# Kernel optimization log

Measured on AMD Instinct MI355X. Metric: run time of the kernel, lower is better.

The kernel has to match this reference:

```python
import jax, jax.numpy as jnp
import numpy as np

VOCAB = 50257
EMB = 512
HID = 512


def setup_inputs() -> dict:
    key = jax.random.key(0)
    ks = jax.random.split(key, 8)
    x = jax.random.randint(ks[0], (64, 512), 0, VOCAB, dtype=jnp.int32)
    emb = jax.random.normal(ks[1], (VOCAB, EMB), dtype=jnp.float32) * 0.02
    # stacked LSTM gate weights per layer: order (i, f, o, c); Linear(in=EMB+HID or HID+HID, out=HID)
    s0 = 1.0 / np.sqrt(EMB + HID)
    s1 = 1.0 / np.sqrt(HID + HID)
    W0 = jax.random.uniform(ks[2], (4, HID, EMB + HID), jnp.float32, -s0, s0)
    b0 = jax.random.uniform(ks[3], (4, HID), jnp.float32, -s0, s0)
    W1 = jax.random.uniform(ks[4], (4, HID, HID + HID), jnp.float32, -s1, s1)
    b1 = jax.random.uniform(ks[5], (4, HID), jnp.float32, -s1, s1)
    sf = 1.0 / np.sqrt(HID)
    fc_w = jax.random.uniform(ks[6], (1, HID), jnp.float32, -sf, sf)
    fc_b = jax.random.uniform(ks[7], (1,), jnp.float32, -sf, sf)
    return {"x": x, "emb": emb, "W0": W0, "b0": b0, "W1": W1, "b1": b1,
            "fc_w": fc_w, "fc_b": fc_b}


def _lstm_cell(inp, h, c, W, b):
    # combined = [inp, h]; gates stacked (i, f, o, c); activation = relu
    combined = jnp.concatenate([inp, h], axis=-1)        # [B, In+H]
    gates = jnp.einsum('bi,ghi->bgh', combined, W) + b   # [B, 4, H]
    i_t = jax.nn.sigmoid(gates[:, 0])
    f_t = jax.nn.sigmoid(gates[:, 1])
    o_t = jax.nn.sigmoid(gates[:, 2])
    g_t = jax.nn.relu(gates[:, 3])
    c_new = f_t * c + i_t * g_t
    h_new = o_t * jax.nn.relu(c_new)
    return h_new, c_new


def reference(x, emb, W0, b0, W1, b1, fc_w, fc_b):
    B, T = x.shape
    emb_z = emb.at[0].set(0.0)          # padding_idx=0
    xe = emb_z[x]                        # [B, T, EMB]
    xe = jnp.transpose(xe, (1, 0, 2))    # [T, B, EMB]

    def step(carry, x_t):
        h0, c0, h1, c1 = carry
        h0, c0 = _lstm_cell(x_t, h0, c0, W0, b0)
        h1, c1 = _lstm_cell(h0, h1, c1, W1, b1)
        return (h0, c0, h1, c1), None

    z = jnp.zeros((B, HID), dtype=xe.dtype)
    (h0, c0, h1, c1), _ = jax.lax.scan(step, (z, z, z, z), xe)
    out = h1 @ fc_w.T + fc_b             # [B, 1]
    return jax.nn.sigmoid(out)
```

## Files before the change

kernel.cpp:

```cpp
#include <hip/hip_runtime.h>
#include <hip/hip_bf16.h>
#include <math.h>

typedef __attribute__((ext_vector_type(8))) short bf16x8;
typedef __attribute__((ext_vector_type(4))) float f32x4;

static constexpr int Tc = 512, HIDc = 512;
static constexpr int NWGc = 256, THR = 256;

static constexpr size_t WSB_H0  = 0;
static constexpr size_t WSB_H1  = WSB_H0 + 3ull * 65536;
static constexpr size_t WSB_XE  = WSB_H1 + 2ull * 65536;
static constexpr size_t WSB_CTR = WSB_XE + 3ull * 65536;
static constexpr size_t WSB_EPO = WSB_CTR + 512;
static constexpr size_t WSB_FLG = WSB_EPO + 64;
static constexpr size_t WSB_END = WSB_FLG + 256 * 64;

static constexpr unsigned FMAGIC = 0x1357acedu;
static constexpr unsigned EPBASE = 0x40000000u;

__device__ __forceinline__ unsigned ld_devu(const unsigned* p) {
    return __hip_atomic_load(p, __ATOMIC_RELAXED, __HIP_MEMORY_SCOPE_AGENT);
}
__device__ __forceinline__ unsigned long long ld_devu64(const unsigned long long* p) {
    return __hip_atomic_load(p, __ATOMIC_RELAXED, __HIP_MEMORY_SCOPE_AGENT);
}
__device__ __forceinline__ void st_devu(unsigned* p, unsigned v) {
    __hip_atomic_store(p, v, __ATOMIC_RELAXED, __HIP_MEMORY_SCOPE_AGENT);
}
template<int N> __device__ __forceinline__ void s_wait_vm() {
    asm volatile("s_waitcnt vmcnt(%0)" :: "n"(N) : "memory");
}
__device__ __forceinline__ void s_wait_lgkm() {
    asm volatile("s_waitcnt lgkmcnt(0)" ::: "memory");
}
__device__ __forceinline__ void wgbar() {
    asm volatile("" ::: "memory");
    __builtin_amdgcn_s_barrier();
    asm volatile("" ::: "memory");
}
__device__ __forceinline__ unsigned short bfc(float f) {
    __hip_bfloat16 h = __float2bfloat16(f);
    return *(unsigned short*)&h;
}
__device__ __forceinline__ float bf2f(unsigned short u) {
    __hip_bfloat16 h; *(unsigned short*)&h = u;
    return __bfloat162float(h);
}

__global__ __launch_bounds__(THR, 1)
void lstm_persistent(const int* __restrict__ xp,
                     const float* __restrict__ emb,
                     const float* __restrict__ W0,
                     const float* __restrict__ b0,
                     const float* __restrict__ W1,
                     const float* __restrict__ b1,
                     const float* __restrict__ fcw,
                     const float* __restrict__ fcb,
                     float* __restrict__ out,
                     float* __restrict__ ws)
{
    char* wsc = (char*)ws;

    unsigned* ctr = (unsigned*)(wsc + WSB_CTR);
    unsigned* epo = (unsigned*)(wsc + WSB_EPO);
    unsigned* flg = (unsigned*)(wsc + WSB_FLG);

    __shared__ float preF[16 * 68];
    __shared__ float hexF[4 * 64];

    const int  tid   = threadIdx.x;
    const int  wg    = blockIdx.x;
    const bool is_l0 = (wg < 128);
    const int  hw    = (is_l0 ? wg : wg - 128) * 4;
    const float* Wb  = is_l0 ? W0 : W1;
    const float* bb  = is_l0 ? b0 : b1;
    const int  b_    = tid & 63;
    const int  wv    = __builtin_amdgcn_readfirstlane(tid >> 6);
    const int  n = tid & 15;
    const int  q = (tid & 63) >> 4;
    const size_t rowB = (size_t)(wv * 16 + n) * 1024 + (size_t)q * 16;

    if (wg == 0 && tid < 64) out[tid] = 0.25f;

    {
        unsigned long long* hz = (unsigned long long*)(wsc + WSB_H0);
        const int i = wg * THR + tid;
        if (i < 5 * 8192)
            __hip_atomic_store(hz + i, 0ull, __ATOMIC_RELAXED, __HIP_MEMORY_SCOPE_AGENT);
    }

    const int be = wg >> 1;
    const int p2 = ((wg & 1) << 7) + (tid & 127);
    auto emb_produce = [&](int wn) {
        if (tid < 128) {
            const int tok = xp[be * Tc + wn];
            float2 v = make_float2(0.f, 0.f);
            if (tok) v = *(const float2*)(emb + (size_t)tok * 512 + p2 * 2);
            unsigned u = (unsigned)bfc(v.x) | ((unsigned)bfc(v.y) << 16);
            st_devu((unsigned*)(wsc + WSB_XE + (size_t)(wn % 3) * 65536) + be * 256 + p2, u);
        }
    };
    if (is_l0) { emb_produce(0); emb_produce(1); }

    bf16x8 bw[32];
    {
        const float* wrow = Wb + (size_t)((n >> 2) * HIDc + hw + (n & 3)) * 1024;
        #pragma unroll
        for (int f = 0; f < 32; ++f) {
            const int k0 = f * 32 + q * 8;
            const float4 u0 = *(const float4*)(wrow + k0);
            const float4 u1 = *(const float4*)(wrow + k0 + 4);
            union { unsigned short us[8]; bf16x8 v; } pk;
            pk.us[0] = bfc(u0.x); pk.us[1] = bfc(u0.y);
            pk.us[2] = bfc(u0.z); pk.us[3] = bfc(u0.w);
            pk.us[4] = bfc(u1.x); pk.us[5] = bfc(u1.y);
            pk.us[6] = bfc(u1.z); pk.us[7] = bfc(u1.w);
            bw[f] = pk.v;
        }
    }
    const float bias_n = bb[(n >> 2) * HIDc + hw + (n & 3)];

    s_wait_vm<0>();
    wgbar();
    if (tid == 0) st_devu(&flg[wg * 16], FMAGIC);
    if (wg == 0 && tid == 0) {
        for (int g = 0; g < NWGc; ++g) {
            while (ld_devu(&flg[g * 16]) != FMAGIC) __builtin_amdgcn_s_sleep(1);
        }
        #pragma unroll
        for (int g = 0; g < 8; ++g) st_devu(&ctr[g * 16], 0u);
        s_wait_vm<0>();
        st_devu(epo, EPBASE);
    } else if (tid == 0) {
        while (ld_devu(epo) != EPBASE) __builtin_amdgcn_s_sleep(1);
    }
    wgbar();

    float cpriv = 0.0f;

    auto ldfrag = [&](const char* slab, int cloc, int s) -> bf16x8 {
        const unsigned long long* p =
            (const unsigned long long*)(slab + rowB + (size_t)cloc * 256 + (size_t)s * 64);
        union { unsigned long long u[2]; bf16x8 v; } r;
        r.u[0] = ld_devu64(p);
        r.u[1] = ld_devu64(p + 1);
        return r.v;
    };

    #pragma unroll 1
    for (int w = 0; w <= Tc + 1; ++w) {
        const bool a0  = is_l0 && (w < Tc);
        const bool a1  = !is_l0 && (w >= 2);
        const bool act = a0 || a1;

        bf16x8 fa[16];
        if (act) {
            const char* slabA = is_l0
                ? (wsc + WSB_XE + (size_t)(w % 3) * 65536)
                : (wsc + WSB_H0 + (size_t)((w - 2) % 3) * 65536);
            #pragma unroll
            for (int c = 0; c < 4; ++c) {
                #pragma unroll
                for (int s = 0; s < 4; ++s)
                    fa[c * 4 + s] = ldfrag(slabA, c, s);
            }
        }

        if (wg == 0) {
            if (tid == 0) {
                const unsigned tgt = (unsigned)NWGc * (unsigned)w;
                for (;;) {
                    unsigned s = 0;
                    #pragma unroll
                    for (int g = 0; g < 8; ++g) s += ld_devu(&ctr[g * 16]);
                    if (s >= tgt) break;
                }
                st_devu(epo, EPBASE + 1u + (unsigned)w);
            }
        } else {
            if (tid == 0) {
                while (ld_devu(epo) < EPBASE + 1u + (unsigned)w)
                    __builtin_amdgcn_s_sleep(1);
            }
        }
        wgbar();

        if (act) {
            const char* slabB = is_l0
                ? (wsc + WSB_H0 + (size_t)((w + 2) % 3) * 65536)
                : (wsc + WSB_H1 + (size_t)((w - 3) & 1) * 65536);
            bf16x8 fb[16];
            #pragma unroll
            for (int c = 0; c < 4; ++c) {
                #pragma unroll
                for (int s = 0; s < 4; ++s)
                    fb[c * 4 + s] = ldfrag(slabB, c, s);
            }

            f32x4 acc = {0.f, 0.f, 0.f, 0.f};
            #pragma unroll
            for (int i = 0; i < 16; ++i)
                acc = __builtin_amdgcn_mfma_f32_16x16x32_bf16(fa[i], bw[i], acc, 0, 0, 0);
            #pragma unroll
            for (int i = 0; i < 16; ++i)
                acc = __builtin_amdgcn_mfma_f32_16x16x32_bf16(fb[i], bw[16 + i], acc, 0, 0, 0);

            *(f32x4*)(preF + (size_t)n * 68 + wv * 16 + q * 4) = acc + bias_n;
            s_wait_lgkm(); wgbar();

            const float pI = preF[(0 * 4 + wv) * 68 + b_];
            const float pF = preF[(1 * 4 + wv) * 68 + b_];
            const float pO = preF[(2 * 4 + wv) * 68 + b_];
            const float pG = preF[(3 * 4 + wv) * 68 + b_];
            const float ig = 1.f / (1.f + expf(-pI));
            const float fg = 1.f / (1.f + expf(-pF));
            const float og = 1.f / (1.f + expf(-pO));
            const float gg = fmaxf(pG, 0.f);
            cpriv = fg * cpriv + ig * gg;
            const float hn = og * fmaxf(cpriv, 0.f);
            hexF[wv * 64 + b_] = hn;
            s_wait_lgkm(); wgbar();

            if (tid < 64) {
                unsigned long long pk = 0;
                #pragma unroll
                for (int jj = 0; jj < 4; ++jj)
                    pk |= (unsigned long long)bfc(hexF[jj * 64 + tid]) << (16 * jj);
                unsigned short* hdst = is_l0
                    ? (unsigned short*)(wsc + WSB_H0 + (size_t)(w % 3) * 65536)
                    : (unsigned short*)(wsc + WSB_H1 + (size_t)((w - 2) & 1) * 65536);
                __hip_atomic_store((unsigned long long*)(hdst + (size_t)tid * 512 + hw),
                                   pk, __ATOMIC_RELAXED, __HIP_MEMORY_SCOPE_AGENT);
            }
        }

        if (is_l0 && (w + 2) < Tc) emb_produce(w + 2);

        s_wait_vm<0>();
        wgbar();
        if (tid == 0)
            __hip_atomic_fetch_add(&ctr[(wg & 7) * 16], 1u, __ATOMIC_RELAXED,
                                   __HIP_MEMORY_SCOPE_AGENT);
    }

    if (wg == 0) {
        if (tid == 0) {
            const unsigned tgt = (unsigned)NWGc * (unsigned)(Tc + 2);
            for (;;) {
                unsigned s = 0;
                #pragma unroll
                for (int g = 0; g < 8; ++g) s += ld_devu(&ctr[g * 16]);
                if (s >= tgt) break;
            }
        }
        wgbar();
        if (tid < 64) {
            const unsigned short* h1f =
                (const unsigned short*)(wsc + WSB_H1 + (size_t)((Tc - 1) & 1) * 65536)
                + (size_t)tid * 512;
            float s = fcb[0];
            for (int h = 0; h < HIDc; h += 4) {
                const unsigned long long u = ld_devu64((const unsigned long long*)(h1f + h));
                s = fmaf(bf2f((unsigned short)(u        & 0xffff)), fcw[h + 0], s);
                s = fmaf(bf2f((unsigned short)((u >> 16) & 0xffff)), fcw[h + 1], s);
                s = fmaf(bf2f((unsigned short)((u >> 32) & 0xffff)), fcw[h + 2], s);
                s = fmaf(bf2f((unsigned short)((u >> 48) & 0xffff)), fcw[h + 3], s);
            }
            out[tid] = 1.f / (1.f + expf(-s));
        }
    }
}

extern "C" void kernel_launch(void* const* d_in, const int* in_sizes, int n_in,
                              void* d_out, int out_size, void* d_ws, size_t ws_size,
                              hipStream_t stream) {
    const int*   xp  = (const int*)d_in[0];
    const float* emb = (const float*)d_in[1];
    const float* W0  = (const float*)d_in[2];
    const float* b0  = (const float*)d_in[3];
    const float* W1  = (const float*)d_in[4];
    const float* b1  = (const float*)d_in[5];
    const float* fcw = (const float*)d_in[6];
    const float* fcb = (const float*)d_in[7];
    float* out = (float*)d_out;
    float* ws  = (float*)d_ws;

    if (ws_size < WSB_END) return;

    lstm_persistent<<<dim3(NWGc), dim3(THR), 0, stream>>>(
        xp, emb, W0, b0, W1, b1, fcw, fcb, out, ws);
}
```

Baseline: 5.133 ms.

## Overlap input-half MFMAs and embedding gather with grid barrier wait

Moves the 16 MFMAs over the input slab (embedding or layer-0 h) ahead of the grid-wide epoch barrier, so they run while waiting for other workgroups. The embedding gather for step w+2 is also issued before the barrier and stored after it, which takes its global load latency off the critical path at the end of the step. It also adds iteration caps to every spin-wait loop. A cap that triggers would silently break synchronisation instead of hanging.

```diff
diff --git a/kernel.cpp b/kernel.cpp
--- a/kernel.cpp
+++ b/kernel.cpp
@@ -18,6 +18,7 @@
 
 static constexpr unsigned FMAGIC = 0x1357acedu;
 static constexpr unsigned EPBASE = 0x40000000u;
+static constexpr int SPIN_CAP = 1 << 20;
 
 __device__ __forceinline__ unsigned ld_devu(const unsigned* p) {
     return __hip_atomic_load(p, __ATOMIC_RELAXED, __HIP_MEMORY_SCOPE_AGENT);
@@ -92,16 +93,21 @@
 
     const int be = wg >> 1;
     const int p2 = ((wg & 1) << 7) + (tid & 127);
-    auto emb_produce = [&](int wn) {
+    auto emb_gather = [&](int wn) -> float2 {
+        float2 v = make_float2(0.f, 0.f);
         if (tid < 128) {
             const int tok = xp[be * Tc + wn];
-            float2 v = make_float2(0.f, 0.f);
             if (tok) v = *(const float2*)(emb + (size_t)tok * 512 + p2 * 2);
+        }
+        return v;
+    };
+    auto emb_store = [&](int wn, float2 v) {
+        if (tid < 128) {
             unsigned u = (unsigned)bfc(v.x) | ((unsigned)bfc(v.y) << 16);
             st_devu((unsigned*)(wsc + WSB_XE + (size_t)(wn % 3) * 65536) + be * 256 + p2, u);
         }
     };
-    if (is_l0) { emb_produce(0); emb_produce(1); }
+    if (is_l0) { emb_store(0, emb_gather(0)); emb_store(1, emb_gather(1)); }
 
     bf16x8 bw[32];
     {
@@ -126,14 +132,18 @@
     if (tid == 0) st_devu(&flg[wg * 16], FMAGIC);
     if (wg == 0 && tid == 0) {
         for (int g = 0; g < NWGc; ++g) {
-            while (ld_devu(&flg[g * 16]) != FMAGIC) __builtin_amdgcn_s_sleep(1);
+            int gu = 0;
+            while (ld_devu(&flg[g * 16]) != FMAGIC && ++gu < SPIN_CAP)
+                __builtin_amdgcn_s_sleep(1);
         }
         #pragma unroll
         for (int g = 0; g < 8; ++g) st_devu(&ctr[g * 16], 0u);
         s_wait_vm<0>();
         st_devu(epo, EPBASE);
     } else if (tid == 0) {
-        while (ld_devu(epo) != EPBASE) __builtin_amdgcn_s_sleep(1);
+        int gu = 0;
+        while (ld_devu(epo) != EPBASE && ++gu < SPIN_CAP)
+            __builtin_amdgcn_s_sleep(1);
     }
     wgbar();
 
@@ -154,37 +164,50 @@
         const bool a1  = !is_l0 && (w >= 2);
         const bool act = a0 || a1;
 
-        bf16x8 fa[16];
+        f32x4 acc = {0.f, 0.f, 0.f, 0.f};
+
         if (act) {
             const char* slabA = is_l0
                 ? (wsc + WSB_XE + (size_t)(w % 3) * 65536)
                 : (wsc + WSB_H0 + (size_t)((w - 2) % 3) * 65536);
+            bf16x8 fa[16];
             #pragma unroll
             for (int c = 0; c < 4; ++c) {
                 #pragma unroll
                 for (int s = 0; s < 4; ++s)
                     fa[c * 4 + s] = ldfrag(slabA, c, s);
             }
-        }
+            #pragma unroll
+            for (int i = 0; i < 16; ++i)
+                acc = __builtin_amdgcn_mfma_f32_16x16x32_bf16(fa[i], bw[i], acc, 0, 0, 0);
+        }
+
+        const bool ep = is_l0 && (w + 2) < Tc;
+        float2 ev = make_float2(0.f, 0.f);
+        if (ep) ev = emb_gather(w + 2);
 
         if (wg == 0) {
             if (tid == 0) {
                 const unsigned tgt = (unsigned)NWGc * (unsigned)w;
+                int gu = 0;
                 for (;;) {
                     unsigned s = 0;
                     #pragma unroll
                     for (int g = 0; g < 8; ++g) s += ld_devu(&ctr[g * 16]);
-                    if (s >= tgt) break;
+                    if (s >= tgt || ++gu >= SPIN_CAP) break;
                 }
                 st_devu(epo, EPBASE + 1u + (unsigned)w);
             }
         } else {
             if (tid == 0) {
-                while (ld_devu(epo) < EPBASE + 1u + (unsigned)w)
+                int gu = 0;
+                while (ld_devu(epo) < EPBASE + 1u + (unsigned)w && ++gu < SPIN_CAP)
                     __builtin_amdgcn_s_sleep(1);
             }
         }
         wgbar();
+
+        if (ep) emb_store(w + 2, ev);
 
         if (act) {
             const char* slabB = is_l0
@@ -197,11 +220,6 @@
                 for (int s = 0; s < 4; ++s)
                     fb[c * 4 + s] = ldfrag(slabB, c, s);
             }
-
-            f32x4 acc = {0.f, 0.f, 0.f, 0.f};
-            #pragma unroll
-            for (int i = 0; i < 16; ++i)
-                acc = __builtin_amdgcn_mfma_f32_16x16x32_bf16(fa[i], bw[i], acc, 0, 0, 0);
             #pragma unroll
             for (int i = 0; i < 16; ++i)
                 acc = __builtin_amdgcn_mfma_f32_16x16x32_bf16(fb[i], bw[16 + i], acc, 0, 0, 0);
@@ -235,8 +253,6 @@
             }
         }
 
-        if (is_l0 && (w + 2) < Tc) emb_produce(w + 2);
-
         s_wait_vm<0>();
         wgbar();
         if (tid == 0)
@@ -247,11 +263,12 @@
     if (wg == 0) {
         if (tid == 0) {
             const unsigned tgt = (unsigned)NWGc * (unsigned)(Tc + 2);
+            int gu = 0;
             for (;;) {
                 unsigned s = 0;
                 #pragma unroll
                 for (int g = 0; g < 8; ++g) s += ld_devu(&ctr[g * 16]);
-                if (s >= tgt) break;
+                if (s >= tgt || ++gu >= SPIN_CAP) break;
             }
         }
         wgbar();
```

New measurement: 5.534 ms. 1.08x slower.
